# Performance work log

Hardware: AMD Instinct MI355X
Metric: run time of the kernel (lower is better)

## Reference

```python
import jax, jax.numpy as jnp
import numpy as np

V, E, H = 50000, 256, 512
BS, SEQ = 64, 200


def setup_inputs() -> dict:
    key = jax.random.key(0)
    ks = jax.random.split(key, 16)
    s = 0.05
    return {
        "input_idx": jax.random.randint(ks[0], (BS,), 0, V),
        "encoded": jax.random.normal(ks[1], (BS, SEQ, 2 * H), jnp.float32),
        "encoded_idx": jax.random.randint(ks[2], (BS, SEQ), 0, V),
        "prev_state": jax.random.normal(ks[3], (BS, H), jnp.float32),
        "weighted": jax.random.normal(ks[4], (BS, 1, 2 * H), jnp.float32),
        "order": 1,
        "embed_W": jax.random.normal(ks[5], (V, E), jnp.float32) * s,
        "Wih": jax.random.normal(ks[6], (3 * H, E + 2 * H), jnp.float32) * s,
        "Whh": jax.random.normal(ks[7], (3 * H, H), jnp.float32) * s,
        "bih": jax.random.normal(ks[8], (3 * H,), jnp.float32) * s,
        "bhh": jax.random.normal(ks[9], (3 * H,), jnp.float32) * s,
        "Ws_W": jax.random.normal(ks[10], (H, 2 * H), jnp.float32) * s,
        "Ws_b": jax.random.normal(ks[11], (H,), jnp.float32) * s,
        "Wo_W": jax.random.normal(ks[12], (V, H), jnp.float32) * s,
        "Wo_b": jax.random.normal(ks[13], (V,), jnp.float32) * s,
        "Wc_W": jax.random.normal(ks[14], (H, 2 * H), jnp.float32) * s,
        "Wc_b": jax.random.normal(ks[15], (H,), jnp.float32) * s,
    }


def reference(input_idx, encoded, encoded_idx, prev_state, weighted, order,
              embed_W, Wih, Whh, bih, bhh, Ws_W, Ws_b, Wo_W, Wo_b, Wc_W, Wc_b):
    bs, seq, _ = encoded.shape
    hidden = Ws_W.shape[0]
    vocab = Wo_W.shape[0]

    if order == 0:
        prev_state = encoded[:, 1] @ Ws_W.T + Ws_b            # [bs, H]
        weighted = jnp.zeros((bs, 1, 2 * hidden), encoded.dtype)

    # GRU single step (batch_first, seq len 1)
    x = jnp.concatenate([embed_W[input_idx], weighted[:, 0, :]], axis=1)  # [bs, E+2H]
    gi = x @ Wih.T + bih                                       # [bs, 3H]
    gh = prev_state @ Whh.T + bhh                              # [bs, 3H]
    i_r, i_z, i_n = jnp.split(gi, 3, axis=1)
    h_r, h_z, h_n = jnp.split(gh, 3, axis=1)
    r = jax.nn.sigmoid(i_r + h_r)
    z = jax.nn.sigmoid(i_z + h_z)
    n = jnp.tanh(i_n + r * h_n)
    state = (1.0 - z) * n + z * prev_state                     # [bs, H]

    # generate and copy scores
    score_g = state @ Wo_W.T + Wo_b                            # [bs, V]
    sc = jnp.tanh(encoded @ Wc_W.T + Wc_b)                     # [bs, seq, H]
    score_c = jnp.einsum('bsh,bh->bs', sc, state)              # [bs, seq]
    enc_mask = jnp.where(encoded_idx == 0, -1000.0, 0.0).astype(score_c.dtype)
    score_c = jnp.tanh(score_c + enc_mask)

    probs = jax.nn.softmax(jnp.concatenate([score_g, score_c], axis=1), axis=1)
    prob_g = probs[:, :vocab]                                  # [bs, V]
    prob_c = probs[:, vocab:]                                  # [bs, seq]

    # scatter-add copy probs into vocab slots
    prob_c_to_g = jnp.zeros((bs, vocab), probs.dtype).at[
        jnp.arange(bs)[:, None], encoded_idx].add(prob_c)
    out = (prob_g + prob_c_to_g)[:, None, :]                   # [bs, 1, V]

    # selective-read attention over positions matching input token
    m = (encoded_idx == input_idx[:, None]).astype(encoded.dtype)  # [bs, seq]
    ssum = m.sum(axis=1, keepdims=True)
    m = jnp.where(ssum > 1, m / ssum, m)
    attn = (prob_c * m)[:, None, :]                            # [bs, 1, seq]
    weighted_out = attn @ encoded                              # [bs, 1, 2H]

    return out, state, weighted_out
```

## Files before the change

kernel.cpp:

```cpp
#include <hip/hip_runtime.h>

#define V 50000
#define E_DIM 256
#define H_DIM 512
#define H2 1024
#define G3 1536
#define BSZ 64
#define SEQ 200
#define KX 1280
#define MROWS 12800
#define NBLK_WO 782

#define XBF_OFF   0
#define H0_OFF    40960
#define H0BF_OFF  73728
#define GI_OFF    90112
#define GH_OFF    188416
#define STBF_OFF  286720
#define WCBF_OFF  303104
#define SC_OFF    565248
#define REDG_OFF  616448
#define RED_OFF   716544
#define ENCBF_OFF 716672

#define OUT_STATE 3200000
#define OUT_W     3232768

typedef __attribute__((ext_vector_type(8))) short bf16x8;
typedef __attribute__((ext_vector_type(4))) float f32x4;

__device__ __forceinline__ float sigmf(float x) { return 1.f / (1.f + __expf(-x)); }

__device__ __forceinline__ ushort f2bf(float f) {
  uint u = __float_as_uint(f);
  uint r = (u + 0x7FFFu + ((u >> 16) & 1u)) >> 16;
  return (ushort)r;
}

__device__ __forceinline__ float tanhfast(float x) {
  float xc = fminf(15.f, fmaxf(-15.f, x));
  float e = __expf(2.f * xc);
  return (e - 1.f) * __builtin_amdgcn_rcpf(e + 1.f);
}

__device__ __forceinline__ bf16x8 cvt8(float4 a, float4 b) {
  union { bf16x8 v; uint u[4]; } r;
  asm("v_cvt_pk_bf16_f32 %0, %1, %2" : "=v"(r.u[0]) : "v"(a.x), "v"(a.y));
  asm("v_cvt_pk_bf16_f32 %0, %1, %2" : "=v"(r.u[1]) : "v"(a.z), "v"(a.w));
  asm("v_cvt_pk_bf16_f32 %0, %1, %2" : "=v"(r.u[2]) : "v"(b.x), "v"(b.y));
  asm("v_cvt_pk_bf16_f32 %0, %1, %2" : "=v"(r.u[3]) : "v"(b.z), "v"(b.w));
  return r.v;
}

__device__ __forceinline__ void gload16(const void* g, void* l) {
  __builtin_amdgcn_global_load_lds(
      (__attribute__((address_space(1))) void*)(g),
      (__attribute__((address_space(3))) void*)(l), 16, 0, 0);
}

__global__ void kprep(const float* __restrict__ Wc_W, ushort* __restrict__ Wc_bf,
                      const float* __restrict__ encoded, ushort* __restrict__ enc_bf,
                      const int* __restrict__ input_idx,
                      const float* __restrict__ prev_state, const float* __restrict__ weighted,
                      const int* __restrict__ order_p, const float* __restrict__ embed_W,
                      const float* __restrict__ Ws_W, const float* __restrict__ Ws_b,
                      ushort* __restrict__ x_bf, float* __restrict__ h0,
                      ushort* __restrict__ h0_bf) {
  int bid = blockIdx.x, tid = threadIdx.x;
  if (bid < 512) {
    int i = bid * 256 + tid;
    float4 v = ((const float4*)Wc_W)[i];
    ushort4 o;
    o.x = f2bf(v.x); o.y = f2bf(v.y); o.z = f2bf(v.z); o.w = f2bf(v.w);
    ((ushort4*)Wc_bf)[i] = o;
    return;
  }
  if (bid < 3712) {
    int base = (bid - 512) * 1024;
#pragma unroll
    for (int j = 0; j < 4; ++j) {
      int i = base + j * 256 + tid;
      float4 v = ((const float4*)encoded)[i];
      ushort4 o;
      o.x = f2bf(v.x); o.y = f2bf(v.y); o.z = f2bf(v.z); o.w = f2bf(v.w);
      ((ushort4*)enc_bf)[i] = o;
    }
    return;
  }
  int b = bid - 3712;
  int order = order_p[0];
  int idx = input_idx[b];
  x_bf[b * KX + tid] = f2bf(embed_W[(size_t)idx * E_DIM + tid]);
  if (order != 0) {
    for (int j = tid; j < H2; j += 256) x_bf[b * KX + E_DIM + j] = f2bf(weighted[b * H2 + j]);
    for (int j = tid; j < H_DIM; j += 256) {
      float v = prev_state[b * H_DIM + j];
      h0[b * H_DIM + j] = v;
      h0_bf[b * H_DIM + j] = f2bf(v);
    }
  } else {
    for (int j = tid; j < H2; j += 256) x_bf[b * KX + E_DIM + j] = 0;
    const float* er = encoded + ((size_t)b * SEQ + 1) * H2;
    for (int j = tid; j < H_DIM; j += 256) {
      float acc = Ws_b[j];
      const float* wr = Ws_W + (size_t)j * H2;
      for (int k = 0; k < H2; ++k) acc = fmaf(er[k], wr[k], acc);
      h0[b * H_DIM + j] = acc;
      h0_bf[b * H_DIM + j] = f2bf(acc);
    }
  }
}

__device__ __forceinline__ void gemm_small(const ushort* __restrict__ Abf,
                                           const float* __restrict__ W,
                                           const float* __restrict__ bias,
                                           float* __restrict__ out, int N, int kdim,
                                           int bid) {
  int tid = threadIdx.x;
  int lane = tid & 63, wv = tid >> 6;
  int l15 = lane & 15, lg = lane >> 4;
  int n0 = (bid * 4 + wv) * 16;
  int col = n0 + l15;
  bool valid = col < N;
  int colc = valid ? col : N - 1;
  f32x4 acc[4];
#pragma unroll
  for (int mt = 0; mt < 4; ++mt) acc[mt] = (f32x4){0.f, 0.f, 0.f, 0.f};
  const float* wrow = W + (size_t)colc * kdim + lg * 8;
  const ushort* arow = Abf + (size_t)l15 * kdim + lg * 8;
#pragma unroll 4
  for (int k0 = 0; k0 < kdim; k0 += 32) {
    float4 w0 = *(const float4*)(wrow + k0);
    float4 w1 = *(const float4*)(wrow + k0 + 4);
    bf16x8 bf = cvt8(w0, w1);
#pragma unroll
    for (int mt = 0; mt < 4; ++mt) {
      bf16x8 af = *(const bf16x8*)(arow + (size_t)mt * 16 * kdim + k0);
      acc[mt] = __builtin_amdgcn_mfma_f32_16x16x32_bf16(af, bf, acc[mt], 0, 0, 0);
    }
  }
  float bv = bias[colc];
  if (valid) {
#pragma unroll
    for (int mt = 0; mt < 4; ++mt)
#pragma unroll
      for (int r = 0; r < 4; ++r)
        out[(size_t)(mt * 16 + lg * 4 + r) * N + col] = acc[mt][r] + bv;
  }
}

__global__ __launch_bounds__(256) void mfma_gates(const ushort* __restrict__ x_bf,
                                                  const float* __restrict__ Wih,
                                                  const float* __restrict__ bih,
                                                  const ushort* __restrict__ h0_bf,
                                                  const float* __restrict__ Whh,
                                                  const float* __restrict__ bhh,
                                                  float* __restrict__ gi, float* __restrict__ gh) {
  if (blockIdx.y == 0)
    gemm_small(x_bf, Wih, bih, gi, G3, KX, blockIdx.x);
  else
    gemm_small(h0_bf, Whh, bhh, gh, G3, H_DIM, blockIdx.x);
}

__global__ void k2_gru(const float* __restrict__ gi, const float* __restrict__ gh,
                       const float* __restrict__ h0, float* __restrict__ state_out,
                       ushort* __restrict__ state_bf) {
  int b = blockIdx.x, j = threadIdx.x;
  float ir = gi[b * G3 + j], iz = gi[b * G3 + H_DIM + j], inn = gi[b * G3 + 2 * H_DIM + j];
  float hr = gh[b * G3 + j], hz = gh[b * G3 + H_DIM + j], hn = gh[b * G3 + 2 * H_DIM + j];
  float r = sigmf(ir + hr);
  float z = sigmf(iz + hz);
  float n = tanhf(inn + r * hn);
  float st = (1.f - z) * n + z * h0[b * H_DIM + j];
  state_out[b * H_DIM + j] = st;
  state_bf[b * H_DIM + j] = f2bf(st);
}

__global__ __launch_bounds__(256) void wo_m97(const ushort* __restrict__ state_bf,
                                              const float* __restrict__ Wo_W,
                                              const float* __restrict__ Wo_b,
                                              float* __restrict__ out,
                                              float* __restrict__ redg) {
  __shared__ char lds[2][24576];
  __shared__ float sm[4][64], ss[4][64];
  int tid = threadIdx.x, lane = tid & 63, wv = tid >> 6;
  int l15 = lane & 15, lg = lane >> 4;
  int bid = blockIdx.x;
  int n0 = bid * 64;
  int colw = n0 + wv * 16 + l15;
  bool vok = colw < V;
  int ccw = vok ? colw : V - 1;
  const ushort* asrc = state_bf + (size_t)(wv * 16 + l15) * H_DIM + lg * 8;
  const float* wsrc = Wo_W + (size_t)ccw * H_DIM + lg * 8;

  f32x4 acc[4];
#pragma unroll
  for (int mf = 0; mf < 4; ++mf) acc[mf] = (f32x4){0.f, 0.f, 0.f, 0.f};

#define STG(buf, it) do {                                               \
    char* d_ = &lds[buf][0];                                            \
    gload16(asrc + (it) * 64,      d_ + (wv * 2 + 0) * 1024);           \
    gload16(asrc + (it) * 64 + 32, d_ + (wv * 2 + 1) * 1024);           \
    gload16(wsrc + (it) * 64,      d_ + 8192 + (wv * 4 + 0) * 1024);    \
    gload16(wsrc + (it) * 64 + 4,  d_ + 8192 + (wv * 4 + 1) * 1024);    \
    gload16(wsrc + (it) * 64 + 32, d_ + 8192 + (wv * 4 + 2) * 1024);    \
    gload16(wsrc + (it) * 64 + 36, d_ + 8192 + (wv * 4 + 3) * 1024);    \
  } while (0)

  STG(0, 0);
  __syncthreads();
#pragma unroll 1
  for (int it = 0; it < 8; ++it) {
    int cur = it & 1;
    if (it < 7) STG(cur ^ 1, it + 1);
    const char* base = &lds[cur][0];
#pragma unroll
    for (int ks = 0; ks < 2; ++ks) {
      float4 w0 = *(const float4*)(base + 8192 + (wv * 4 + ks * 2 + 0) * 1024 + lane * 16);
      float4 w1 = *(const float4*)(base + 8192 + (wv * 4 + ks * 2 + 1) * 1024 + lane * 16);
      bf16x8 wf = cvt8(w0, w1);
#pragma unroll
      for (int mf = 0; mf < 4; ++mf) {
        bf16x8 a = *(const bf16x8*)(base + (mf * 2 + ks) * 1024 + lane * 16);
        acc[mf] = __builtin_amdgcn_mfma_f32_16x16x32_bf16(a, wf, acc[mf], 0, 0, 0);
      }
    }
    __syncthreads();
  }
#undef STG

  float bv = Wo_b[ccw];
#pragma unroll
  for (int mf = 0; mf < 4; ++mf)
#pragma unroll
    for (int r = 0; r < 4; ++r) {
      size_t row = (size_t)(mf * 16 + lg * 4 + r) * V;
      if (vok) out[row + colw] = acc[mf][r] + bv;
    }
#pragma unroll
  for (int mf = 0; mf < 4; ++mf)
#pragma unroll
    for (int r = 0; r < 4; ++r) {
      float a0 = vok ? acc[mf][r] + bv : -1e30f;
      float mx = a0;
#pragma unroll
      for (int off = 1; off < 16; off <<= 1) mx = fmaxf(mx, __shfl_xor(mx, off, 64));
      float e = vok ? __expf(a0 - mx) : 0.f;
#pragma unroll
      for (int off = 1; off < 16; off <<= 1) e += __shfl_xor(e, off, 64);
      if (l15 == 0) {
        sm[wv][mf * 16 + lg * 4 + r] = mx;
        ss[wv][mf * 16 + lg * 4 + r] = e;
      }
    }
  __syncthreads();
  if (tid < 64) {
    float M = -1e30f, S = 0.f;
#pragma unroll
    for (int w = 0; w < 4; ++w) {
      float m2 = sm[w][tid], s2 = ss[w][tid];
      float mn = fmaxf(M, m2);
      S = S * __expf(M - mn) + s2 * __expf(m2 - mn);
      M = mn;
    }
    redg[((size_t)tid * NBLK_WO + bid) * 2] = M;
    redg[((size_t)tid * NBLK_WO + bid) * 2 + 1] = S;
  }
}

__global__ __launch_bounds__(256) void k4_mfma9(const ushort* __restrict__ enc_bf,
                                                const ushort* __restrict__ Wc_bf,
                                                const float* __restrict__ Wc_b,
                                                const float* __restrict__ state,
                                                float* __restrict__ scpart) {
  __shared__ char lds[2][24576];
  __shared__ float sred[4][64];
  int tid = threadIdx.x, lane = tid & 63, wv = tid >> 6;
  int l15 = lane & 15, lg = lane >> 4;
  int bid = blockIdx.x;
  int mtile = bid >> 2, ntile = bid & 3;
  int m0 = mtile * 64, n0 = ntile * 128;

  const ushort* asrc = enc_bf + (size_t)(m0 + wv * 16 + l15) * H2 + lg * 8;
  const ushort* bsrc0 = Wc_bf + (size_t)(n0 + (wv * 2 + 0) * 16 + l15) * H2 + lg * 8;
  const ushort* bsrc1 = Wc_bf + (size_t)(n0 + (wv * 2 + 1) * 16 + l15) * H2 + lg * 8;

  f32x4 acc[4][2];
#pragma unroll
  for (int mf = 0; mf < 4; ++mf)
#pragma unroll
    for (int nf = 0; nf < 2; ++nf) acc[mf][nf] = (f32x4){0.f, 0.f, 0.f, 0.f};

#define STG(buf, it) do {                                              \
    char* d_ = &lds[buf][0];                                           \
    gload16(asrc + (it) * 64,       d_ + (wv * 2 + 0) * 1024);         \
    gload16(asrc + (it) * 64 + 32,  d_ + (wv * 2 + 1) * 1024);         \
    gload16(bsrc0 + (it) * 64,      d_ + 8192 + (wv * 4 + 0) * 1024);  \
    gload16(bsrc0 + (it) * 64 + 32, d_ + 8192 + (wv * 4 + 1) * 1024);  \
    gload16(bsrc1 + (it) * 64,      d_ + 8192 + (wv * 4 + 2) * 1024);  \
    gload16(bsrc1 + (it) * 64 + 32, d_ + 8192 + (wv * 4 + 3) * 1024);  \
  } while (0)

  STG(0, 0);
  __syncthreads();
#pragma unroll 1
  for (int it = 0; it < 16; ++it) {
    int cur = it & 1;
    if (it < 15) STG(cur ^ 1, it + 1);
    const char* base = &lds[cur][0];
#pragma unroll
    for (int ks = 0; ks < 2; ++ks) {
      bf16x8 b0 = *(const bf16x8*)(base + 8192 + (wv * 4 + ks) * 1024 + lane * 16);
      bf16x8 b1 = *(const bf16x8*)(base + 8192 + (wv * 4 + 2 + ks) * 1024 + lane * 16);
#pragma unroll
      for (int mf = 0; mf < 4; ++mf) {
        bf16x8 a = *(const bf16x8*)(base + (mf * 2 + ks) * 1024 + lane * 16);
        acc[mf][0] = __builtin_amdgcn_mfma_f32_16x16x32_bf16(a, b0, acc[mf][0], 0, 0, 0);
        acc[mf][1] = __builtin_amdgcn_mfma_f32_16x16x32_bf16(a, b1, acc[mf][1], 0, 0, 0);
      }
    }
    __syncthreads();
  }
#undef STG

  float pv[4][4];
#pragma unroll
  for (int mf = 0; mf < 4; ++mf)
#pragma unroll
    for (int r = 0; r < 4; ++r) pv[mf][r] = 0.f;
#pragma unroll
  for (int nfl = 0; nfl < 2; ++nfl) {
    int n = n0 + (wv * 2 + nfl) * 16 + l15;
    float bias = Wc_b[n];
#pragma unroll
    for (int mf = 0; mf < 4; ++mf) {
      int mrow = m0 + mf * 16 + lg * 4;
#pragma unroll
      for (int r = 0; r < 4; ++r) {
        int b = (mrow + r) / SEQ;
        pv[mf][r] += tanhfast(acc[mf][nfl][r] + bias) * state[b * H_DIM + n];
      }
    }
  }
#pragma unroll
  for (int off = 1; off < 16; off <<= 1)
#pragma unroll
    for (int mf = 0; mf < 4; ++mf)
#pragma unroll
      for (int r = 0; r < 4; ++r) pv[mf][r] += __shfl_xor(pv[mf][r], off, 64);
  if (l15 == 0) {
#pragma unroll
    for (int mf = 0; mf < 4; ++mf)
#pragma unroll
      for (int r = 0; r < 4; ++r) sred[wv][mf * 16 + lg * 4 + r] = pv[mf][r];
  }
  __syncthreads();
  if (tid < 64) {
    float s = sred[0][tid] + sred[1][tid] + sred[2][tid] + sred[3][tid];
    scpart[(size_t)ntile * MROWS + m0 + tid] = s;
  }
}

__global__ void kred(const float* __restrict__ redg, const float* __restrict__ scpart,
                     const int* __restrict__ eidx, float* __restrict__ red) {
  int b = blockIdx.x, tid = threadIdx.x;
  float m = -1e30f, s = 0.f;
  for (int i = tid; i < NBLK_WO; i += 256) {
    float m2 = redg[((size_t)b * NBLK_WO + i) * 2];
    float s2 = redg[((size_t)b * NBLK_WO + i) * 2 + 1];
    float mn = fmaxf(m, m2);
    s = s * __expf(m - mn) + s2 * __expf(m2 - mn);
    m = mn;
  }
  for (int i = tid; i < SEQ; i += 256) {
    int idx = b * SEQ + i;
    int ei = eidx[idx];
    float scv = scpart[idx] + scpart[MROWS + idx] + scpart[2 * MROWS + idx] +
                scpart[3 * MROWS + idx];
    float sc = tanhf(scv + (ei == 0 ? -1000.f : 0.f));
    float mn = fmaxf(m, sc);
    s = s * __expf(m - mn) + __expf(sc - mn);
    m = mn;
  }
  __shared__ float ms[256], ssh[256];
  ms[tid] = m; ssh[tid] = s;
  __syncthreads();
  for (int off = 128; off > 0; off >>= 1) {
    if (tid < off) {
      float m2 = ms[tid + off], s2 = ssh[tid + off];
      float mn = fmaxf(ms[tid], m2);
      ssh[tid] = ssh[tid] * __expf(ms[tid] - mn) + s2 * __expf(m2 - mn);
      ms[tid] = mn;
    }
    __syncthreads();
  }
  if (tid == 0) {
    red[b * 2] = ms[0];
    red[b * 2 + 1] = ssh[0];
  }
}

__global__ void k7_probs(float* __restrict__ sg, const float* __restrict__ red) {
  int i = blockIdx.x * 256 + threadIdx.x;
  int b = i / 12500;
  float mm = red[b * 2], rd = 1.f / red[b * 2 + 1];
  float4* p = (float4*)sg;
  float4 v = p[i];
  v.x = __expf(v.x - mm) * rd;
  v.y = __expf(v.y - mm) * rd;
  v.z = __expf(v.z - mm) * rd;
  v.w = __expf(v.w - mm) * rd;
  p[i] = v;
}

__global__ void k8_copy(const float* __restrict__ scpart, const int* __restrict__ eidx,
                        const int* __restrict__ input_idx, const float* __restrict__ red,
                        const float* __restrict__ encoded, float* __restrict__ out,
                        float* __restrict__ wout) {
  int b = blockIdx.x, tid = threadIdx.x;
  __shared__ float att_s[SEQ];
  __shared__ int cnt_s[256];
  float mm = red[b * 2], rd = 1.f / red[b * 2 + 1];
  int inp = input_idx[b];
  int cnt = 0;
  for (int s = tid; s < SEQ; s += 256) {
    int idx = b * SEQ + s;
    int ei = eidx[idx];
    float scv = scpart[idx] + scpart[MROWS + idx] + scpart[2 * MROWS + idx] +
                scpart[3 * MROWS + idx];
    float sc = tanhf(scv + (ei == 0 ? -1000.f : 0.f));
    float p = __expf(sc - mm) * rd;
    bool mt = (ei == inp);
    att_s[s] = mt ? p : 0.f;
    cnt += mt ? 1 : 0;
    atomicAdd(&out[(size_t)b * V + ei], p);
  }
  cnt_s[tid] = cnt;
  __syncthreads();
  for (int off = 128; off > 0; off >>= 1) {
    if (tid < off) cnt_s[tid] += cnt_s[tid + off];
    __syncthreads();
  }
  int c = cnt_s[0];
  float scale = (c > 1) ? 1.f / (float)c : 1.f;
  float w0 = 0, w1 = 0, w2 = 0, w3 = 0;
  for (int s = 0; s < SEQ; ++s) {
    float a = att_s[s];
    if (a != 0.f) {
      const float* er = encoded + ((size_t)b * SEQ + s) * H2;
      w0 += a * er[tid];
      w1 += a * er[tid + 256];
      w2 += a * er[tid + 512];
      w3 += a * er[tid + 768];
    }
  }
  wout[b * H2 + tid] = w0 * scale;
  wout[b * H2 + tid + 256] = w1 * scale;
  wout[b * H2 + tid + 512] = w2 * scale;
  wout[b * H2 + tid + 768] = w3 * scale;
}

extern "C" void kernel_launch(void* const* d_in, const int* in_sizes, int n_in,
                              void* d_out, int out_size, void* d_ws, size_t ws_size,
                              hipStream_t stream) {
  const int* input_idx = (const int*)d_in[0];
  const float* encoded = (const float*)d_in[1];
  const int* encoded_idx = (const int*)d_in[2];
  const float* prev_state = (const float*)d_in[3];
  const float* weighted = (const float*)d_in[4];
  const int* order_p = (const int*)d_in[5];
  const float* embed_W = (const float*)d_in[6];
  const float* Wih = (const float*)d_in[7];
  const float* Whh = (const float*)d_in[8];
  const float* bih = (const float*)d_in[9];
  const float* bhh = (const float*)d_in[10];
  const float* Ws_W = (const float*)d_in[11];
  const float* Ws_b = (const float*)d_in[12];
  const float* Wo_W = (const float*)d_in[13];
  const float* Wo_b = (const float*)d_in[14];
  const float* Wc_W = (const float*)d_in[15];
  const float* Wc_b = (const float*)d_in[16];

  float* ws = (float*)d_ws;
  float* out = (float*)d_out;
  ushort* x_bf = (ushort*)(ws + XBF_OFF);
  float* h0 = ws + H0_OFF;
  ushort* h0_bf = (ushort*)(ws + H0BF_OFF);
  float* gi = ws + GI_OFF;
  float* gh = ws + GH_OFF;
  ushort* state_bf = (ushort*)(ws + STBF_OFF);
  ushort* Wc_bf = (ushort*)(ws + WCBF_OFF);
  float* scpart = ws + SC_OFF;
  float* redg = ws + REDG_OFF;
  float* red = ws + RED_OFF;
  ushort* enc_bf = (ushort*)(ws + ENCBF_OFF);
  float* state = out + OUT_STATE;
  float* wout = out + OUT_W;

  kprep<<<3776, 256, 0, stream>>>(Wc_W, Wc_bf, encoded, enc_bf, input_idx, prev_state,
                                  weighted, order_p, embed_W, Ws_W, Ws_b, x_bf, h0, h0_bf);
  mfma_gates<<<dim3(24, 2), 256, 0, stream>>>(x_bf, Wih, bih, h0_bf, Whh, bhh, gi, gh);
  k2_gru<<<64, 512, 0, stream>>>(gi, gh, h0, state, state_bf);
  wo_m97<<<NBLK_WO, 256, 0, stream>>>(state_bf, Wo_W, Wo_b, out, redg);
  k4_mfma9<<<800, 256, 0, stream>>>(enc_bf, Wc_bf, Wc_b, state, scpart);
  kred<<<64, 256, 0, stream>>>(redg, scpart, encoded_idx, red);
  k7_probs<<<3125, 256, 0, stream>>>(out, red);
  k8_copy<<<64, 256, 0, stream>>>(scpart, encoded_idx, input_idx, red, encoded, out, wout);
}
```

Measured before the change: 164.2 us.

## Fuse Wo projection and copy-score GEMM into one interleaved launch

Merges the vocab-projection GEMM kernel and the encoder copy-score GEMM kernel into a single launch of 1600 blocks. Odd blocks do Wo tiles and even blocks do Wc tiles, so the memory-bound Wo stream and the compute-heavier Wc GEMM run at the same time. This removes one launch boundary and the tail of each kernel. The cost is a divergent branch per block, plus register and LDS pressure set by the larger of the two paths.

```diff
diff --git a/kernel.cpp b/kernel.cpp
--- a/kernel.cpp
+++ b/kernel.cpp
@@ -176,120 +176,119 @@
   state_bf[b * H_DIM + j] = f2bf(st);
 }
 
-__global__ __launch_bounds__(256) void wo_m97(const ushort* __restrict__ state_bf,
-                                              const float* __restrict__ Wo_W,
-                                              const float* __restrict__ Wo_b,
-                                              float* __restrict__ out,
-                                              float* __restrict__ redg) {
+__global__ __launch_bounds__(256) void fused_big(const ushort* __restrict__ enc_bf,
+                                                 const ushort* __restrict__ Wc_bf,
+                                                 const float* __restrict__ Wc_b,
+                                                 const float* __restrict__ state,
+                                                 const ushort* __restrict__ state_bf,
+                                                 const float* __restrict__ Wo_W,
+                                                 const float* __restrict__ Wo_b,
+                                                 float* __restrict__ out,
+                                                 float* __restrict__ redg,
+                                                 float* __restrict__ scpart) {
   __shared__ char lds[2][24576];
-  __shared__ float sm[4][64], ss[4][64];
+  __shared__ float s0buf[4][64], s1buf[4][64];
   int tid = threadIdx.x, lane = tid & 63, wv = tid >> 6;
   int l15 = lane & 15, lg = lane >> 4;
   int bid = blockIdx.x;
-  int n0 = bid * 64;
-  int colw = n0 + wv * 16 + l15;
-  bool vok = colw < V;
-  int ccw = vok ? colw : V - 1;
-  const ushort* asrc = state_bf + (size_t)(wv * 16 + l15) * H_DIM + lg * 8;
-  const float* wsrc = Wo_W + (size_t)ccw * H_DIM + lg * 8;
-
-  f32x4 acc[4];
-#pragma unroll
-  for (int mf = 0; mf < 4; ++mf) acc[mf] = (f32x4){0.f, 0.f, 0.f, 0.f};
-
-#define STG(buf, it) do {                                               \
-    char* d_ = &lds[buf][0];                                            \
-    gload16(asrc + (it) * 64,      d_ + (wv * 2 + 0) * 1024);           \
-    gload16(asrc + (it) * 64 + 32, d_ + (wv * 2 + 1) * 1024);           \
-    gload16(wsrc + (it) * 64,      d_ + 8192 + (wv * 4 + 0) * 1024);    \
-    gload16(wsrc + (it) * 64 + 4,  d_ + 8192 + (wv * 4 + 1) * 1024);    \
-    gload16(wsrc + (it) * 64 + 32, d_ + 8192 + (wv * 4 + 2) * 1024);    \
-    gload16(wsrc + (it) * 64 + 36, d_ + 8192 + (wv * 4 + 3) * 1024);    \
+
+  if (bid & 1) {
+    int wt = bid >> 1;
+    if (wt >= NBLK_WO) return;
+    int n0 = wt * 64;
+    int colw = n0 + wv * 16 + l15;
+    bool vok = colw < V;
+    int ccw = vok ? colw : V - 1;
+    const ushort* asrc = state_bf + (size_t)(wv * 16 + l15) * H_DIM + lg * 8;
+    const float* wsrc = Wo_W + (size_t)ccw * H_DIM + lg * 8;
+
+    f32x4 acc[4];
+#pragma unroll
+    for (int mf = 0; mf < 4; ++mf) acc[mf] = (f32x4){0.f, 0.f, 0.f, 0.f};
+
+#define STGW(buf, it) do {                                               \
+    char* d_ = &lds[buf][0];                                             \
+    gload16(asrc + (it) * 64,      d_ + (wv * 2 + 0) * 1024);            \
+    gload16(asrc + (it) * 64 + 32, d_ + (wv * 2 + 1) * 1024);            \
+    gload16(wsrc + (it) * 64,      d_ + 8192 + (wv * 4 + 0) * 1024);     \
+    gload16(wsrc + (it) * 64 + 4,  d_ + 8192 + (wv * 4 + 1) * 1024);     \
+    gload16(wsrc + (it) * 64 + 32, d_ + 8192 + (wv * 4 + 2) * 1024);     \
+    gload16(wsrc + (it) * 64 + 36, d_ + 8192 + (wv * 4 + 3) * 1024);     \
   } while (0)
 
-  STG(0, 0);
-  __syncthreads();
+    STGW(0, 0);
+    __syncthreads();
 #pragma unroll 1
-  for (int it = 0; it < 8; ++it) {
-    int cur = it & 1;
-    if (it < 7) STG(cur ^ 1, it + 1);
-    const char* base = &lds[cur][0];
-#pragma unroll
-    for (int ks = 0; ks < 2; ++ks) {
-      float4 w0 = *(const float4*)(base + 8192 + (wv * 4 + ks * 2 + 0) * 1024 + lane * 16);
-      float4 w1 = *(const float4*)(base + 8192 + (wv * 4 + ks * 2 + 1) * 1024 + lane * 16);
-      bf16x8 wf = cvt8(w0, w1);
-#pragma unroll
-      for (int mf = 0; mf < 4; ++mf) {
-        bf16x8 a = *(const bf16x8*)(base + (mf * 2 + ks) * 1024 + lane * 16);
-        acc[mf] = __builtin_amdgcn_mfma_f32_16x16x32_bf16(a, wf, acc[mf], 0, 0, 0);
+    for (int it = 0; it < 8; ++it) {
+      int cur = it & 1;
+      if (it < 7) STGW(cur ^ 1, it + 1);
+      const char* base = &lds[cur][0];
+#pragma unroll
+      for (int ks = 0; ks < 2; ++ks) {
+        float4 w0 = *(const float4*)(base + 8192 + (wv * 4 + ks * 2 + 0) * 1024 + lane * 16);
+        float4 w1 = *(const float4*)(base + 8192 + (wv * 4 + ks * 2 + 1) * 1024 + lane * 16);
+        bf16x8 wf = cvt8(w0, w1);
+#pragma unroll
+        for (int mf = 0; mf < 4; ++mf) {
+          bf16x8 a = *(const bf16x8*)(base + (mf * 2 + ks) * 1024 + lane * 16);
+          acc[mf] = __builtin_amdgcn_mfma_f32_16x16x32_bf16(a, wf, acc[mf], 0, 0, 0);
+        }
       }
-    }
+      __syncthreads();
+    }
+#undef STGW
+
+    float bv = Wo_b[ccw];
+#pragma unroll
+    for (int mf = 0; mf < 4; ++mf)
+#pragma unroll
+      for (int r = 0; r < 4; ++r) {
+        size_t row = (size_t)(mf * 16 + lg * 4 + r) * V;
+        if (vok) out[row + colw] = acc[mf][r] + bv;
+      }
+#pragma unroll
+    for (int mf = 0; mf < 4; ++mf)
+#pragma unroll
+      for (int r = 0; r < 4; ++r) {
+        float a0 = vok ? acc[mf][r] + bv : -1e30f;
+        float mx = a0;
+#pragma unroll
+        for (int off = 1; off < 16; off <<= 1) mx = fmaxf(mx, __shfl_xor(mx, off, 64));
+        float e = vok ? __expf(a0 - mx) : 0.f;
+#pragma unroll
+        for (int off = 1; off < 16; off <<= 1) e += __shfl_xor(e, off, 64);
+        if (l15 == 0) {
+          s0buf[wv][mf * 16 + lg * 4 + r] = mx;
+          s1buf[wv][mf * 16 + lg * 4 + r] = e;
+        }
+      }
     __syncthreads();
-  }
-#undef STG
-
-  float bv = Wo_b[ccw];
-#pragma unroll
-  for (int mf = 0; mf < 4; ++mf)
-#pragma unroll
-    for (int r = 0; r < 4; ++r) {
-      size_t row = (size_t)(mf * 16 + lg * 4 + r) * V;
-      if (vok) out[row + colw] = acc[mf][r] + bv;
-    }
-#pragma unroll
-  for (int mf = 0; mf < 4; ++mf)
-#pragma unroll
-    for (int r = 0; r < 4; ++r) {
-      float a0 = vok ? acc[mf][r] + bv : -1e30f;
-      float mx = a0;
-#pragma unroll
-      for (int off = 1; off < 16; off <<= 1) mx = fmaxf(mx, __shfl_xor(mx, off, 64));
-      float e = vok ? __expf(a0 - mx) : 0.f;
-#pragma unroll
-      for (int off = 1; off < 16; off <<= 1) e += __shfl_xor(e, off, 64);
-      if (l15 == 0) {
-        sm[wv][mf * 16 + lg * 4 + r] = mx;
-        ss[wv][mf * 16 + lg * 4 + r] = e;
+    if (tid < 64) {
+      float M = -1e30f, S = 0.f;
+#pragma unroll
+      for (int w = 0; w < 4; ++w) {
+        float m2 = s0buf[w][tid], s2 = s1buf[w][tid];
+        float mn = fmaxf(M, m2);
+        S = S * __expf(M - mn) + s2 * __expf(m2 - mn);
+        M = mn;
       }
-    }
-  __syncthreads();
-  if (tid < 64) {
-    float M = -1e30f, S = 0.f;
-#pragma unroll
-    for (int w = 0; w < 4; ++w) {
-      float m2 = sm[w][tid], s2 = ss[w][tid];
-      float mn = fmaxf(M, m2);
-      S = S * __expf(M - mn) + s2 * __expf(m2 - mn);
-      M = mn;
-    }
-    redg[((size_t)tid * NBLK_WO + bid) * 2] = M;
-    redg[((size_t)tid * NBLK_WO + bid) * 2 + 1] = S;
-  }
-}
-
-__global__ __launch_bounds__(256) void k4_mfma9(const ushort* __restrict__ enc_bf,
-                                                const ushort* __restrict__ Wc_bf,
-                                                const float* __restrict__ Wc_b,
-                                                const float* __restrict__ state,
-                                                float* __restrict__ scpart) {
-  __shared__ char lds[2][24576];
-  __shared__ float sred[4][64];
-  int tid = threadIdx.x, lane = tid & 63, wv = tid >> 6;
-  int l15 = lane & 15, lg = lane >> 4;
-  int bid = blockIdx.x;
-  int mtile = bid >> 2, ntile = bid & 3;
-  int m0 = mtile * 64, n0 = ntile * 128;
-
-  const ushort* asrc = enc_bf + (size_t)(m0 + wv * 16 + l15) * H2 + lg * 8;
-  const ushort* bsrc0 = Wc_bf + (size_t)(n0 + (wv * 2 + 0) * 16 + l15) * H2 + lg * 8;
-  const ushort* bsrc1 = Wc_bf + (size_t)(n0 + (wv * 2 + 1) * 16 + l15) * H2 + lg * 8;
-
-  f32x4 acc[4][2];
-#pragma unroll
-  for (int mf = 0; mf < 4; ++mf)
-#pragma unroll
-    for (int nf = 0; nf < 2; ++nf) acc[mf][nf] = (f32x4){0.f, 0.f, 0.f, 0.f};
+      redg[((size_t)tid * NBLK_WO + wt) * 2] = M;
+      redg[((size_t)tid * NBLK_WO + wt) * 2 + 1] = S;
+    }
+  } else {
+    int kt = bid >> 1;
+    int mtile = kt >> 2, ntile = kt & 3;
+    int m0 = mtile * 64, n0 = ntile * 128;
+
+    const ushort* asrc = enc_bf + (size_t)(m0 + wv * 16 + l15) * H2 + lg * 8;
+    const ushort* bsrc0 = Wc_bf + (size_t)(n0 + (wv * 2 + 0) * 16 + l15) * H2 + lg * 8;
+    const ushort* bsrc1 = Wc_bf + (size_t)(n0 + (wv * 2 + 1) * 16 + l15) * H2 + lg * 8;
+
+    f32x4 acc[4][2];
+#pragma unroll
+    for (int mf = 0; mf < 4; ++mf)
+#pragma unroll
+      for (int nf = 0; nf < 2; ++nf) acc[mf][nf] = (f32x4){0.f, 0.f, 0.f, 0.f};
 
 #define STG(buf, it) do {                                              \
     char* d_ = &lds[buf][0];                                           \
@@ -301,63 +300,64 @@
     gload16(bsrc1 + (it) * 64 + 32, d_ + 8192 + (wv * 4 + 3) * 1024);  \
   } while (0)
 
-  STG(0, 0);
-  __syncthreads();
+    STG(0, 0);
+    __syncthreads();
 #pragma unroll 1
-  for (int it = 0; it < 16; ++it) {
-    int cur = it & 1;
-    if (it < 15) STG(cur ^ 1, it + 1);
-    const char* base = &lds[cur][0];
-#pragma unroll
-    for (int ks = 0; ks < 2; ++ks) {
-      bf16x8 b0 = *(const bf16x8*)(base + 8192 + (wv * 4 + ks) * 1024 + lane * 16);
-      bf16x8 b1 = *(const bf16x8*)(base + 8192 + (wv * 4 + 2 + ks) * 1024 + lane * 16);
+    for (int it = 0; it < 16; ++it) {
+      int cur = it & 1;
+      if (it < 15) STG(cur ^ 1, it + 1);
+      const char* base = &lds[cur][0];
+#pragma unroll
+      for (int ks = 0; ks < 2; ++ks) {
+        bf16x8 b0 = *(const bf16x8*)(base + 8192 + (wv * 4 + ks) * 1024 + lane * 16);
+        bf16x8 b1 = *(const bf16x8*)(base + 8192 + (wv * 4 + 2 + ks) * 1024 + lane * 16);
+#pragma unroll
+        for (int mf = 0; mf < 4; ++mf) {
+          bf16x8 a = *(const bf16x8*)(base + (mf * 2 + ks) * 1024 + lane * 16);
+          acc[mf][0] = __builtin_amdgcn_mfma_f32_16x16x32_bf16(a, b0, acc[mf][0], 0, 0, 0);
+          acc[mf][1] = __builtin_amdgcn_mfma_f32_16x16x32_bf16(a, b1, acc[mf][1], 0, 0, 0);
+        }
+      }
+      __syncthreads();
+    }
+#undef STG
+
+    float pv[4][4];
+#pragma unroll
+    for (int mf = 0; mf < 4; ++mf)
+#pragma unroll
+      for (int r = 0; r < 4; ++r) pv[mf][r] = 0.f;
+#pragma unroll
+    for (int nfl = 0; nfl < 2; ++nfl) {
+      int n = n0 + (wv * 2 + nfl) * 16 + l15;
+      float bias = Wc_b[n];
 #pragma unroll
       for (int mf = 0; mf < 4; ++mf) {
-        bf16x8 a = *(const bf16x8*)(base + (mf * 2 + ks) * 1024 + lane * 16);
-        acc[mf][0] = __builtin_amdgcn_mfma_f32_16x16x32_bf16(a, b0, acc[mf][0], 0, 0, 0);
-        acc[mf][1] = __builtin_amdgcn_mfma_f32_16x16x32_bf16(a, b1, acc[mf][1], 0, 0, 0);
+        int mrow = m0 + mf * 16 + lg * 4;
+#pragma unroll
+        for (int r = 0; r < 4; ++r) {
+          int b = (mrow + r) / SEQ;
+          pv[mf][r] += tanhfast(acc[mf][nfl][r] + bias) * state[b * H_DIM + n];
+        }
       }
     }
+#pragma unroll
+    for (int off = 1; off < 16; off <<= 1)
+#pragma unroll
+      for (int mf = 0; mf < 4; ++mf)
+#pragma unroll
+        for (int r = 0; r < 4; ++r) pv[mf][r] += __shfl_xor(pv[mf][r], off, 64);
+    if (l15 == 0) {
+#pragma unroll
+      for (int mf = 0; mf < 4; ++mf)
+#pragma unroll
+        for (int r = 0; r < 4; ++r) s0buf[wv][mf * 16 + lg * 4 + r] = pv[mf][r];
+    }
     __syncthreads();
-  }
-#undef STG
-
-  float pv[4][4];
-#pragma unroll
-  for (int mf = 0; mf < 4; ++mf)
-#pragma unroll
-    for (int r = 0; r < 4; ++r) pv[mf][r] = 0.f;
-#pragma unroll
-  for (int nfl = 0; nfl < 2; ++nfl) {
-    int n = n0 + (wv * 2 + nfl) * 16 + l15;
-    float bias = Wc_b[n];
-#pragma unroll
-    for (int mf = 0; mf < 4; ++mf) {
-      int mrow = m0 + mf * 16 + lg * 4;
-#pragma unroll
-      for (int r = 0; r < 4; ++r) {
-        int b = (mrow + r) / SEQ;
-        pv[mf][r] += tanhfast(acc[mf][nfl][r] + bias) * state[b * H_DIM + n];
-      }
-    }
-  }
-#pragma unroll
-  for (int off = 1; off < 16; off <<= 1)
-#pragma unroll
-    for (int mf = 0; mf < 4; ++mf)
-#pragma unroll
-      for (int r = 0; r < 4; ++r) pv[mf][r] += __shfl_xor(pv[mf][r], off, 64);
-  if (l15 == 0) {
-#pragma unroll
-    for (int mf = 0; mf < 4; ++mf)
-#pragma unroll
-      for (int r = 0; r < 4; ++r) sred[wv][mf * 16 + lg * 4 + r] = pv[mf][r];
-  }
-  __syncthreads();
-  if (tid < 64) {
-    float s = sred[0][tid] + sred[1][tid] + sred[2][tid] + sred[3][tid];
-    scpart[(size_t)ntile * MROWS + m0 + tid] = s;
+    if (tid < 64) {
+      float s = s0buf[0][tid] + s0buf[1][tid] + s0buf[2][tid] + s0buf[3][tid];
+      scpart[(size_t)ntile * MROWS + m0 + tid] = s;
+    }
   }
 }
 
@@ -501,8 +501,8 @@
                                   weighted, order_p, embed_W, Ws_W, Ws_b, x_bf, h0, h0_bf);
   mfma_gates<<<dim3(24, 2), 256, 0, stream>>>(x_bf, Wih, bih, h0_bf, Whh, bhh, gi, gh);
   k2_gru<<<64, 512, 0, stream>>>(gi, gh, h0, state, state_bf);
-  wo_m97<<<NBLK_WO, 256, 0, stream>>>(state_bf, Wo_W, Wo_b, out, redg);
-  k4_mfma9<<<800, 256, 0, stream>>>(enc_bf, Wc_bf, Wc_b, state, scpart);
+  fused_big<<<1600, 256, 0, stream>>>(enc_bf, Wc_bf, Wc_b, state, state_bf,
+                                      Wo_W, Wo_b, out, redg, scpart);
   kred<<<64, 256, 0, stream>>>(redg, scpart, encoded_idx, red);
   k7_probs<<<3125, 256, 0, stream>>>(out, red);
   k8_copy<<<64, 256, 0, stream>>>(scpart, encoded_idx, input_idx, red, encoded, out, wout);
```

New measurement: 160.2 us. 2.4% less time.
